# Kernel optimization log

Hardware: AMD Instinct MI355X
Metric: run time of the kernel (lower is better)

Reference implementation:

```python
import jax, jax.numpy as jnp
import numpy as np

N_NODES = 50000
N_EDGES = 600000
D_FEAT = 128
HIDDEN = 128
N_CLASSES = 40
K_HOPS = 2


def setup_inputs() -> dict:
    key = jax.random.key(0)
    k_x, k_e, k_w1, k_b1, k_w2, k_b2 = jax.random.split(key, 6)
    x = jax.random.normal(k_x, (N_NODES, D_FEAT), dtype=jnp.float32)
    edge_index = jax.random.randint(k_e, (2, N_EDGES), 0, N_NODES, dtype=jnp.int64)
    # SGConv linear (applied after K-hop propagation) and classifier, Glorot-ish init
    W_sgc = jax.random.normal(k_w1, (D_FEAT, HIDDEN), dtype=jnp.float32) / np.sqrt(D_FEAT)
    b_sgc = jnp.zeros((HIDDEN,), dtype=jnp.float32)
    W_cls = jax.random.normal(k_w2, (HIDDEN, N_CLASSES), dtype=jnp.float32) / np.sqrt(HIDDEN)
    b_cls = jnp.zeros((N_CLASSES,), dtype=jnp.float32)
    return {"x": x, "edge_index": edge_index, "W_sgc": W_sgc, "b_sgc": b_sgc,
            "W_cls": W_cls, "b_cls": b_cls}


def _gcn_norm(edge_index, num_nodes):
    # Add self-loops (PyG SGConv default), compute symmetric GCN normalization.
    loops = jnp.arange(num_nodes, dtype=edge_index.dtype)
    src = jnp.concatenate([edge_index[0], loops])  # [E+N]
    dst = jnp.concatenate([edge_index[1], loops])  # [E+N]
    deg = jax.ops.segment_sum(jnp.ones_like(dst, dtype=jnp.float32), dst,
                              num_segments=num_nodes)
    dinv = jnp.where(deg > 0, jax.lax.rsqrt(deg), 0.0)
    norm = dinv[src] * dinv[dst]  # [E+N]
    return src, dst, norm


def reference(x, edge_index, W_sgc, b_sgc, W_cls, b_cls):
    num_nodes = x.shape[0]
    src, dst, norm = _gcn_norm(edge_index, num_nodes)
    h = x
    for _ in range(K_HOPS):  # K-hop propagation: h <- D^-1/2 (A+I) D^-1/2 h
        h = jax.ops.segment_sum(norm[:, None] * h[src], dst, num_segments=num_nodes)
    h = h @ W_sgc + b_sgc          # SGConv's trailing linear
    # F.dropout with training=False is identity (inference); skip.
    out = h @ W_cls + b_cls        # classifier
    return out
```

## Files before the change

### kernel.cpp

```cpp
#include <hip/hip_runtime.h>
#include <hip/hip_fp16.h>

#define N_NODES 50000
#define N_EDGES 600000
#define D 128
#define NC 40
#define BUCKET_CAP 96
#define NPART 8
#define PART_SZ (N_NODES / NPART)
#define ZERO_BLKS ((N_NODES / 4 + 255) / 256)
#define FUSE_ELEMS (D * NC + NC)
#define FUSE_BLKS ((FUSE_ELEMS + 255) / 256)
#define E4 (N_EDGES / 4)
#define FILLB_PER_PART ((E4 + 255) / 256)
#define FILLB (FILLB_PER_PART * NPART)
#define PROJB ((N_NODES + 63) / 64)

typedef int v4i __attribute__((ext_vector_type(4)));
typedef _Float16 hf2 __attribute__((ext_vector_type(2)));

struct alignas(16) H8 { __half2 h[4]; };
struct alignas(8)  H4 { __half2 h[2]; };
struct alignas(16) HV4 { hf2 h[4]; };

__device__ __forceinline__ float4 h4f(H4 v) {
    float2 p = __half22float2(v.h[0]), q = __half22float2(v.h[1]);
    return make_float4(p.x, p.y, q.x, q.y);
}


__global__ void k_zero_fuse(int4* __restrict__ cnt4,
                            const float* __restrict__ Wsgc, const float* __restrict__ bsgc,
                            const float* __restrict__ Wcls, const float* __restrict__ bcls,
                            float* __restrict__ Wf, float* __restrict__ bf) {
    if (blockIdx.x < ZERO_BLKS) {
        int i = blockIdx.x * 256 + threadIdx.x;
        if (i < N_NODES / 4) cnt4[i] = make_int4(0, 0, 0, 0);
    } else {
        int idx = (blockIdx.x - ZERO_BLKS) * 256 + threadIdx.x;
        if (idx < D * NC) {
            int k = idx / NC, c = idx % NC;
            float acc = 0.f;
            for (int j = 0; j < D; j++) acc += Wsgc[k * D + j] * Wcls[j * NC + c];
            Wf[idx] = acc;
        } else if (idx < FUSE_ELEMS) {
            int c = idx - D * NC;
            float acc = bcls[c];
            for (int j = 0; j < D; j++) acc += bsgc[j] * Wcls[j * NC + c];
            bf[c] = acc;
        }
    }
}


__global__ void k_fill(const v4i* __restrict__ src4, const v4i* __restrict__ dst4,
                       int* __restrict__ cnt, int* __restrict__ bucket) {
    int part = blockIdx.x & (NPART - 1);
    int bip  = blockIdx.x >> 3;
    int lo = part * PART_SZ, hi = lo + PART_SZ;
    int i = bip * 256 + threadIdx.x;
    if (i >= E4) return;
    v4i d = __builtin_nontemporal_load(&dst4[i]);
    v4i s = __builtin_nontemporal_load(&src4[i]);
#define FILL_ONE(dd, ss)                                              \
    if ((dd) >= lo && (dd) < hi) {                                    \
        int pos = atomicAdd(&cnt[dd], 1);                             \
        if (pos < BUCKET_CAP) bucket[(size_t)(dd) * BUCKET_CAP + pos] = (ss); \
    }
    FILL_ONE(d.x, s.x)
    FILL_ONE(d.y, s.y)
    FILL_ONE(d.z, s.z)
    FILL_ONE(d.w, s.w)
#undef FILL_ONE
}


__global__ __launch_bounds__(320) void k_proj(const float* __restrict__ x,
                                              const float* __restrict__ Wf,
                                              const int* __restrict__ cnt,
                                              __half* __restrict__ u0) {
    __shared__ hf2 sW[64][40];
    __shared__ hf2 sX[64][65];
    int t = threadIdx.x;
    for (int i = t; i < 64 * 40; i += 320) {
        int k2 = i / 40, c = i - k2 * 40;
        hf2 w;
        w.x = (_Float16)Wf[(2 * k2) * NC + c];
        w.y = (_Float16)Wf[(2 * k2 + 1) * NC + c];
        sW[k2][c] = w;
    }
    int base = blockIdx.x * 64;
    int rows = N_NODES - base;
    if (rows > 64) rows = 64;
    const float2* xs = reinterpret_cast<const float2*>(x + (size_t)base * D);
    for (int i = t; i < rows * 64; i += 320) {
        int r = i >> 6, k2 = i & 63;
        float2 v = xs[(size_t)r * 64 + k2];
        hf2 h;
        h.x = (_Float16)v.x;
        h.y = (_Float16)v.y;
        sX[r][k2] = h;
    }
    __syncthreads();
    int lane = t & 63;
    int wv = t >> 6;
    int c0 = wv * 8;
    int node = base + lane;
    if (node >= N_NODES) return;
    float a0 = 0.f, a1 = 0.f, a2 = 0.f, a3 = 0.f;
    float a4 = 0.f, a5 = 0.f, a6 = 0.f, a7 = 0.f;
#pragma unroll 8
    for (int k2 = 0; k2 < 64; k2++) {
        hf2 hx = sX[lane][k2];
        HV4 wa = *reinterpret_cast<const HV4*>(&sW[k2][c0]);
        HV4 wb = *reinterpret_cast<const HV4*>(&sW[k2][c0 + 4]);
#if __has_builtin(__builtin_amdgcn_fdot2)
        a0 = __builtin_amdgcn_fdot2(hx, wa.h[0], a0, false);
        a1 = __builtin_amdgcn_fdot2(hx, wa.h[1], a1, false);
        a2 = __builtin_amdgcn_fdot2(hx, wa.h[2], a2, false);
        a3 = __builtin_amdgcn_fdot2(hx, wa.h[3], a3, false);
        a4 = __builtin_amdgcn_fdot2(hx, wb.h[0], a4, false);
        a5 = __builtin_amdgcn_fdot2(hx, wb.h[1], a5, false);
        a6 = __builtin_amdgcn_fdot2(hx, wb.h[2], a6, false);
        a7 = __builtin_amdgcn_fdot2(hx, wb.h[3], a7, false);
#else
        float xl = (float)hx.x, xh = (float)hx.y;
        a0 += xl * (float)wa.h[0].x + xh * (float)wa.h[0].y;
        a1 += xl * (float)wa.h[1].x + xh * (float)wa.h[1].y;
        a2 += xl * (float)wa.h[2].x + xh * (float)wa.h[2].y;
        a3 += xl * (float)wa.h[3].x + xh * (float)wa.h[3].y;
        a4 += xl * (float)wb.h[0].x + xh * (float)wb.h[0].y;
        a5 += xl * (float)wb.h[1].x + xh * (float)wb.h[1].y;
        a6 += xl * (float)wb.h[2].x + xh * (float)wb.h[2].y;
        a7 += xl * (float)wb.h[3].x + xh * (float)wb.h[3].y;
#endif
    }
    float s = rsqrtf((float)cnt[node] + 1.0f);
    H8 o;
    o.h[0] = __floats2half2_rn(s * a0, s * a1);
    o.h[1] = __floats2half2_rn(s * a2, s * a3);
    o.h[2] = __floats2half2_rn(s * a4, s * a5);
    o.h[3] = __floats2half2_rn(s * a6, s * a7);
    *reinterpret_cast<H8*>(u0 + (size_t)node * NC + c0) = o;
}


template <int MODE>
__global__ void k_pull(const int* __restrict__ cnt, const int* __restrict__ bucket,
                       const __half* __restrict__ hin, void* __restrict__ houtv,
                       const float* __restrict__ bias) {
    int wave = threadIdx.x >> 6;
    int lane = threadIdx.x & 63;
    int g = lane / 10;
    int l = lane - g * 10;
    int node = blockIdx.x * 24 + wave * 6 + g;
    if (g >= 6 || node >= N_NODES) return;
    int f = l << 2;
    int c = cnt[node];
    int n = c < BUCKET_CAP ? c : BUCKET_CAP;
    float4 acc = h4f(*reinterpret_cast<const H4*>(hin + (size_t)node * NC + f));
    const int* bk = bucket + (size_t)node * BUCKET_CAP;
    int j = 0;
    for (; j + 4 <= n; j += 4) {
        int s0 = bk[j], s1 = bk[j + 1], s2 = bk[j + 2], s3 = bk[j + 3];
        float4 v0 = h4f(*reinterpret_cast<const H4*>(hin + (size_t)s0 * NC + f));
        float4 v1 = h4f(*reinterpret_cast<const H4*>(hin + (size_t)s1 * NC + f));
        float4 v2 = h4f(*reinterpret_cast<const H4*>(hin + (size_t)s2 * NC + f));
        float4 v3 = h4f(*reinterpret_cast<const H4*>(hin + (size_t)s3 * NC + f));
        acc.x += v0.x + v1.x + v2.x + v3.x;
        acc.y += v0.y + v1.y + v2.y + v3.y;
        acc.z += v0.z + v1.z + v2.z + v3.z;
        acc.w += v0.w + v1.w + v2.w + v3.w;
    }
    for (; j < n; j++) {
        int s0 = bk[j];
        float4 v0 = h4f(*reinterpret_cast<const H4*>(hin + (size_t)s0 * NC + f));
        acc.x += v0.x; acc.y += v0.y; acc.z += v0.z; acc.w += v0.w;
    }
    float s = (MODE == 0) ? 1.0f / ((float)c + 1.0f)
                          : rsqrtf((float)c + 1.0f);
    acc.x *= s; acc.y *= s; acc.z *= s; acc.w *= s;
    if (MODE == 0) {
        __half* ho = (__half*)houtv;
        H4 o;
        o.h[0] = __floats2half2_rn(acc.x, acc.y);
        o.h[1] = __floats2half2_rn(acc.z, acc.w);
        *reinterpret_cast<H4*>(ho + (size_t)node * NC + f) = o;
    } else {
        float* ho = (float*)houtv;
        float4 b = *reinterpret_cast<const float4*>(bias + f);
        acc.x += b.x; acc.y += b.y; acc.z += b.z; acc.w += b.w;
        *reinterpret_cast<float4*>(ho + (size_t)node * NC + f) = acc;
    }
}


extern "C" void kernel_launch(void* const* d_in, const int* in_sizes, int n_in,
                              void* d_out, int out_size, void* d_ws, size_t ws_size,
                              hipStream_t stream) {
    const float* x    = (const float*)d_in[0];
    const int*   ei   = (const int*)d_in[1];
    const float* Wsgc = (const float*)d_in[2];
    const float* bsgc = (const float*)d_in[3];
    const float* Wcls = (const float*)d_in[4];
    const float* bcls = (const float*)d_in[5];
    float* out = (float*)d_out;

    const v4i* src4 = (const v4i*)ei;
    const v4i* dst4 = (const v4i*)(ei + N_EDGES);

    char* ws = (char*)d_ws;
    size_t off = 0;
    auto alloc = [&](size_t bytes) -> void* {
        void* p = ws + off;
        off += (bytes + 255) & ~255ull;
        return p;
    };
    int*    cnt    = (int*)alloc((size_t)N_NODES * 4);
    int*    bucket = (int*)alloc((size_t)N_NODES * BUCKET_CAP * 4);
    __half* u0     = (__half*)alloc((size_t)N_NODES * NC * 2);
    __half* u1     = (__half*)alloc((size_t)N_NODES * NC * 2);
    float*  Wf     = (float*)alloc((size_t)D * NC * 4);
    float*  bf     = (float*)alloc((size_t)NC * 4);

    const int pull_blks = (N_NODES + 23) / 24;

    k_zero_fuse<<<ZERO_BLKS + FUSE_BLKS, 256, 0, stream>>>((int4*)cnt, Wsgc, bsgc,
                                                           Wcls, bcls, Wf, bf);
    k_fill<<<FILLB, 256, 0, stream>>>(src4, dst4, cnt, bucket);
    k_proj<<<PROJB, 320, 0, stream>>>(x, Wf, cnt, u0);
    k_pull<0><<<pull_blks, 256, 0, stream>>>(cnt, bucket, u0, (void*)u1, nullptr);
    k_pull<1><<<pull_blks, 256, 0, stream>>>(cnt, bucket, u1, (void*)out, bf);
}
```

Before: 91.20 us.

## Pack edges to 16-bit pairs and co-schedule bucket fill with projection

```diff
diff --git a/kernel.cpp b/kernel.cpp
--- a/kernel.cpp
+++ b/kernel.cpp
@@ -8,13 +8,17 @@
 #define BUCKET_CAP 96
 #define NPART 8
 #define PART_SZ (N_NODES / NPART)
+#define E4 (N_EDGES / 4)
+#define FUSE_ELEMS (D * NC + NC)
+
 #define ZERO_BLKS ((N_NODES / 4 + 255) / 256)
-#define FUSE_ELEMS (D * NC + NC)
 #define FUSE_BLKS ((FUSE_ELEMS + 255) / 256)
-#define E4 (N_EDGES / 4)
-#define FILLB_PER_PART ((E4 + 255) / 256)
-#define FILLB (FILLB_PER_PART * NPART)
+#define CMP_BLKS ((E4 + 255) / 256)
+#define K0B (ZERO_BLKS + FUSE_BLKS + CMP_BLKS)
+
+#define FILLB 1024
 #define PROJB ((N_NODES + 63) / 64)
+#define K1B (FILLB + PROJB)
 
 typedef int v4i __attribute__((ext_vector_type(4)));
 typedef _Float16 hf2 __attribute__((ext_vector_type(2)));
@@ -29,15 +33,18 @@
 }
 
 
-__global__ void k_zero_fuse(int4* __restrict__ cnt4,
-                            const float* __restrict__ Wsgc, const float* __restrict__ bsgc,
-                            const float* __restrict__ Wcls, const float* __restrict__ bcls,
-                            float* __restrict__ Wf, float* __restrict__ bf) {
-    if (blockIdx.x < ZERO_BLKS) {
-        int i = blockIdx.x * 256 + threadIdx.x;
+__global__ void k_prep(int4* __restrict__ cnt4,
+                       const float* __restrict__ Wsgc, const float* __restrict__ bsgc,
+                       const float* __restrict__ Wcls, const float* __restrict__ bcls,
+                       float* __restrict__ Wf, float* __restrict__ bf,
+                       const v4i* __restrict__ src4, const v4i* __restrict__ dst4,
+                       v4i* __restrict__ packed4) {
+    int b = blockIdx.x, t = threadIdx.x;
+    if (b < ZERO_BLKS) {
+        int i = b * 256 + t;
         if (i < N_NODES / 4) cnt4[i] = make_int4(0, 0, 0, 0);
-    } else {
-        int idx = (blockIdx.x - ZERO_BLKS) * 256 + threadIdx.x;
+    } else if (b < ZERO_BLKS + FUSE_BLKS) {
+        int idx = (b - ZERO_BLKS) * 256 + t;
         if (idx < D * NC) {
             int k = idx / NC, c = idx % NC;
             float acc = 0.f;
@@ -49,39 +56,52 @@
             for (int j = 0; j < D; j++) acc += bsgc[j] * Wcls[j * NC + c];
             bf[c] = acc;
         }
-    }
-}
-
-
-__global__ void k_fill(const v4i* __restrict__ src4, const v4i* __restrict__ dst4,
-                       int* __restrict__ cnt, int* __restrict__ bucket) {
-    int part = blockIdx.x & (NPART - 1);
-    int bip  = blockIdx.x >> 3;
-    int lo = part * PART_SZ, hi = lo + PART_SZ;
-    int i = bip * 256 + threadIdx.x;
-    if (i >= E4) return;
-    v4i d = __builtin_nontemporal_load(&dst4[i]);
-    v4i s = __builtin_nontemporal_load(&src4[i]);
-#define FILL_ONE(dd, ss)                                              \
-    if ((dd) >= lo && (dd) < hi) {                                    \
-        int pos = atomicAdd(&cnt[dd], 1);                             \
-        if (pos < BUCKET_CAP) bucket[(size_t)(dd) * BUCKET_CAP + pos] = (ss); \
-    }
-    FILL_ONE(d.x, s.x)
-    FILL_ONE(d.y, s.y)
-    FILL_ONE(d.z, s.z)
-    FILL_ONE(d.w, s.w)
-#undef FILL_ONE
-}
-
-
-__global__ __launch_bounds__(320) void k_proj(const float* __restrict__ x,
-                                              const float* __restrict__ Wf,
-                                              const int* __restrict__ cnt,
-                                              __half* __restrict__ u0) {
+    } else {
+        int i = (b - ZERO_BLKS - FUSE_BLKS) * 256 + t;
+        if (i < E4) {
+            v4i d = __builtin_nontemporal_load(&dst4[i]);
+            v4i s = __builtin_nontemporal_load(&src4[i]);
+            v4i p;
+            p.x = (int)(((unsigned)d.x << 16) | (unsigned)s.x);
+            p.y = (int)(((unsigned)d.y << 16) | (unsigned)s.y);
+            p.z = (int)(((unsigned)d.z << 16) | (unsigned)s.z);
+            p.w = (int)(((unsigned)d.w << 16) | (unsigned)s.w);
+            packed4[i] = p;
+        }
+    }
+}
+
+
+__global__ __launch_bounds__(320) void k_fill_proj(
+    const v4i* __restrict__ packed4, int* __restrict__ cnt,
+    unsigned short* __restrict__ bucket,
+    const float* __restrict__ x, const float* __restrict__ Wf,
+    __half* __restrict__ z) {
     __shared__ hf2 sW[64][40];
     __shared__ hf2 sX[64][65];
-    int t = threadIdx.x;
+    int t = threadIdx.x, b = blockIdx.x;
+    if (b < FILLB) {
+        int part = b & (NPART - 1);
+        int bip  = b >> 3;
+        int lo = part * PART_SZ, hi = lo + PART_SZ;
+        const int stride = (FILLB >> 3) * 320;
+        for (int i = bip * 320 + t; i < E4; i += stride) {
+            v4i p = __builtin_nontemporal_load(&packed4[i]);
+#define FO(pp)                                                             \
+            {                                                              \
+                int d = (int)(((unsigned)(pp)) >> 16);                     \
+                if (d >= lo && d < hi) {                                   \
+                    int pos = atomicAdd(&cnt[d], 1);                       \
+                    if (pos < BUCKET_CAP)                                  \
+                        bucket[(size_t)d * BUCKET_CAP + pos] =             \
+                            (unsigned short)((pp) & 0xFFFF);               \
+                }                                                          \
+            }
+            FO(p.x) FO(p.y) FO(p.z) FO(p.w)
+#undef FO
+        }
+        return;
+    }
     for (int i = t; i < 64 * 40; i += 320) {
         int k2 = i / 40, c = i - k2 * 40;
         hf2 w;
@@ -89,7 +109,7 @@
         w.y = (_Float16)Wf[(2 * k2 + 1) * NC + c];
         sW[k2][c] = w;
     }
-    int base = blockIdx.x * 64;
+    int base = (b - FILLB) * 64;
     int rows = N_NODES - base;
     if (rows > 64) rows = 64;
     const float2* xs = reinterpret_cast<const float2*>(x + (size_t)base * D);
@@ -135,18 +155,18 @@
         a7 += xl * (float)wb.h[3].x + xh * (float)wb.h[3].y;
 #endif
     }
-    float s = rsqrtf((float)cnt[node] + 1.0f);
     H8 o;
-    o.h[0] = __floats2half2_rn(s * a0, s * a1);
-    o.h[1] = __floats2half2_rn(s * a2, s * a3);
-    o.h[2] = __floats2half2_rn(s * a4, s * a5);
-    o.h[3] = __floats2half2_rn(s * a6, s * a7);
-    *reinterpret_cast<H8*>(u0 + (size_t)node * NC + c0) = o;
+    o.h[0] = __floats2half2_rn(a0, a1);
+    o.h[1] = __floats2half2_rn(a2, a3);
+    o.h[2] = __floats2half2_rn(a4, a5);
+    o.h[3] = __floats2half2_rn(a6, a7);
+    *reinterpret_cast<H8*>(z + (size_t)node * NC + c0) = o;
 }
 
 
 template <int MODE>
-__global__ void k_pull(const int* __restrict__ cnt, const int* __restrict__ bucket,
+__global__ void k_pull(const int* __restrict__ cnt,
+                       const unsigned short* __restrict__ bucket,
                        const __half* __restrict__ hin, void* __restrict__ houtv,
                        const float* __restrict__ bias) {
     int wave = threadIdx.x >> 6;
@@ -158,8 +178,10 @@
     int f = l << 2;
     int c = cnt[node];
     int n = c < BUCKET_CAP ? c : BUCKET_CAP;
+    float di = rsqrtf((float)c + 1.0f);
     float4 acc = h4f(*reinterpret_cast<const H4*>(hin + (size_t)node * NC + f));
-    const int* bk = bucket + (size_t)node * BUCKET_CAP;
+    if (MODE == 0) { acc.x *= di; acc.y *= di; acc.z *= di; acc.w *= di; }
+    const unsigned short* bk = bucket + (size_t)node * BUCKET_CAP;
     int j = 0;
     for (; j + 4 <= n; j += 4) {
         int s0 = bk[j], s1 = bk[j + 1], s2 = bk[j + 2], s3 = bk[j + 3];
@@ -167,29 +189,40 @@
         float4 v1 = h4f(*reinterpret_cast<const H4*>(hin + (size_t)s1 * NC + f));
         float4 v2 = h4f(*reinterpret_cast<const H4*>(hin + (size_t)s2 * NC + f));
         float4 v3 = h4f(*reinterpret_cast<const H4*>(hin + (size_t)s3 * NC + f));
-        acc.x += v0.x + v1.x + v2.x + v3.x;
-        acc.y += v0.y + v1.y + v2.y + v3.y;
-        acc.z += v0.z + v1.z + v2.z + v3.z;
-        acc.w += v0.w + v1.w + v2.w + v3.w;
+        if (MODE == 0) {
+            float w0 = rsqrtf((float)cnt[s0] + 1.0f);
+            float w1 = rsqrtf((float)cnt[s1] + 1.0f);
+            float w2 = rsqrtf((float)cnt[s2] + 1.0f);
+            float w3 = rsqrtf((float)cnt[s3] + 1.0f);
+            acc.x += w0 * v0.x + w1 * v1.x + w2 * v2.x + w3 * v3.x;
+            acc.y += w0 * v0.y + w1 * v1.y + w2 * v2.y + w3 * v3.y;
+            acc.z += w0 * v0.z + w1 * v1.z + w2 * v2.z + w3 * v3.z;
+            acc.w += w0 * v0.w + w1 * v1.w + w2 * v2.w + w3 * v3.w;
+        } else {
+            acc.x += v0.x + v1.x + v2.x + v3.x;
+            acc.y += v0.y + v1.y + v2.y + v3.y;
+            acc.z += v0.z + v1.z + v2.z + v3.z;
+            acc.w += v0.w + v1.w + v2.w + v3.w;
+        }
     }
     for (; j < n; j++) {
         int s0 = bk[j];
         float4 v0 = h4f(*reinterpret_cast<const H4*>(hin + (size_t)s0 * NC + f));
-        acc.x += v0.x; acc.y += v0.y; acc.z += v0.z; acc.w += v0.w;
-    }
-    float s = (MODE == 0) ? 1.0f / ((float)c + 1.0f)
-                          : rsqrtf((float)c + 1.0f);
-    acc.x *= s; acc.y *= s; acc.z *= s; acc.w *= s;
+        float w0 = (MODE == 0) ? rsqrtf((float)cnt[s0] + 1.0f) : 1.0f;
+        acc.x += w0 * v0.x; acc.y += w0 * v0.y; acc.z += w0 * v0.z; acc.w += w0 * v0.w;
+    }
     if (MODE == 0) {
+        float sc = di * di;
         __half* ho = (__half*)houtv;
         H4 o;
-        o.h[0] = __floats2half2_rn(acc.x, acc.y);
-        o.h[1] = __floats2half2_rn(acc.z, acc.w);
+        o.h[0] = __floats2half2_rn(sc * acc.x, sc * acc.y);
+        o.h[1] = __floats2half2_rn(sc * acc.z, sc * acc.w);
         *reinterpret_cast<H4*>(ho + (size_t)node * NC + f) = o;
     } else {
         float* ho = (float*)houtv;
         float4 b = *reinterpret_cast<const float4*>(bias + f);
-        acc.x += b.x; acc.y += b.y; acc.z += b.z; acc.w += b.w;
+        acc.x = di * acc.x + b.x; acc.y = di * acc.y + b.y;
+        acc.z = di * acc.z + b.z; acc.w = di * acc.w + b.w;
         *reinterpret_cast<float4*>(ho + (size_t)node * NC + f) = acc;
     }
 }
@@ -216,19 +249,19 @@
         off += (bytes + 255) & ~255ull;
         return p;
     };
-    int*    cnt    = (int*)alloc((size_t)N_NODES * 4);
-    int*    bucket = (int*)alloc((size_t)N_NODES * BUCKET_CAP * 4);
-    __half* u0     = (__half*)alloc((size_t)N_NODES * NC * 2);
-    __half* u1     = (__half*)alloc((size_t)N_NODES * NC * 2);
-    float*  Wf     = (float*)alloc((size_t)D * NC * 4);
-    float*  bf     = (float*)alloc((size_t)NC * 4);
+    int*            cnt    = (int*)alloc((size_t)N_NODES * 4);
+    unsigned short* bucket = (unsigned short*)alloc((size_t)N_NODES * BUCKET_CAP * 2);
+    v4i*            packed = (v4i*)alloc((size_t)N_EDGES * 4);
+    __half*         z      = (__half*)alloc((size_t)N_NODES * NC * 2);
+    __half*         u1     = (__half*)alloc((size_t)N_NODES * NC * 2);
+    float*          Wf     = (float*)alloc((size_t)D * NC * 4);
+    float*          bf     = (float*)alloc((size_t)NC * 4);
 
     const int pull_blks = (N_NODES + 23) / 24;
 
-    k_zero_fuse<<<ZERO_BLKS + FUSE_BLKS, 256, 0, stream>>>((int4*)cnt, Wsgc, bsgc,
-                                                           Wcls, bcls, Wf, bf);
-    k_fill<<<FILLB, 256, 0, stream>>>(src4, dst4, cnt, bucket);
-    k_proj<<<PROJB, 320, 0, stream>>>(x, Wf, cnt, u0);
-    k_pull<0><<<pull_blks, 256, 0, stream>>>(cnt, bucket, u0, (void*)u1, nullptr);
+    k_prep<<<K0B, 256, 0, stream>>>((int4*)cnt, Wsgc, bsgc, Wcls, bcls, Wf, bf,
+                                    src4, dst4, (v4i*)packed);
+    k_fill_proj<<<K1B, 320, 0, stream>>>((const v4i*)packed, cnt, bucket, x, Wf, z);
+    k_pull<0><<<pull_blks, 256, 0, stream>>>(cnt, bucket, z, (void*)u1, nullptr);
     k_pull<1><<<pull_blks, 256, 0, stream>>>(cnt, bucket, u1, (void*)out, bf);
 }
```

Result: faster. 85.65 us (-6.1%).
